# Kernel tuning notes

Hardware: AMD Instinct MI355X
Metric: run time of the kernel (lower is better)

## Reference

```python
import jax, jax.numpy as jnp
import numpy as np

N = 1_000_000
D = 128
B = 1024  # number of graphs in the batch


def setup_inputs() -> dict:
    key = jax.random.key(0)
    k1, k2, k3 = jax.random.split(key, 3)
    feat = jax.random.normal(k1, (N, D), dtype=jnp.float32)
    w_gate = jax.random.normal(k2, (D, 1), dtype=jnp.float32) * 0.02
    b_gate = jnp.zeros((1,), dtype=jnp.float32)
    segment_ids = jnp.sort(jax.random.randint(k3, (N,), 0, B, dtype=jnp.int32))
    return {"feat": feat, "w_gate": w_gate, "b_gate": b_gate,
            "segment_ids": segment_ids}


def reference(feat, w_gate, b_gate, segment_ids):
    # gate_nn: Linear(D, 1) -> per-node scalar score
    gate = (feat @ w_gate + b_gate)[:, 0]                      # [N]
    # softmax_nodes: per-graph (segment) numerically stable softmax
    seg_max = jax.ops.segment_max(gate, segment_ids, num_segments=B)   # [B]
    e = jnp.exp(gate - seg_max[segment_ids])                   # [N]
    seg_sum = jax.ops.segment_sum(e, segment_ids, num_segments=B)      # [B]
    alpha = e / seg_sum[segment_ids]                           # [N]
    # sum_nodes of feat * gate: weighted per-graph readout
    readout = jax.ops.segment_sum(feat * alpha[:, None], segment_ids,
                                  num_segments=B)              # [B, D]
    return readout, alpha[:, None]
```

## Files before the change

kernel.cpp:

```cpp
#include <hip/hip_runtime.h>
#include <math.h>

__global__ __launch_bounds__(256) void k_segstart(
        const int* __restrict__ seg, int* __restrict__ segstart, int N, int B) {
    int i = blockIdx.x * blockDim.x + threadIdx.x;
    if (i >= N) return;
    int s = seg[i];
    int p = (i == 0) ? -1 : seg[i - 1];
    for (int bb = p + 1; bb <= s; ++bb) segstart[bb] = i;
    if (i == N - 1)
        for (int bb = s + 1; bb <= B; ++bb) segstart[bb] = N;
}

__global__ __launch_bounds__(256) void k_pool(
        const float* __restrict__ feat, const float* __restrict__ w,
        const float* __restrict__ bptr, const int* __restrict__ segstart,
        float* __restrict__ gbuf, float* __restrict__ Mbuf,
        float* __restrict__ invbuf, float* __restrict__ readout) {
    int b = blockIdx.x;
    int start = segstart[b], end = segstart[b + 1];
    int t = threadIdx.x, rg = t >> 5, cl = t & 31;

    const float4 w4 = ((const float4*)w)[cl];
    const float bias = bptr[0];
    const float4* featv = (const float4*)feat;

    float m = -INFINITY, s = 0.0f;
    float4 acc = make_float4(0.0f, 0.0f, 0.0f, 0.0f);

    const int n0 = start + rg;

#define LDROW(dst, row)                                                       \
    dst = ((row) < end) ? featv[(size_t)(row) * 32 + cl]                      \
                        : make_float4(0.0f, 0.0f, 0.0f, 0.0f)

    float4 f0, f1, f2, f3;
    LDROW(f0, n0);
    LDROW(f1, n0 + 8);
    LDROW(f2, n0 + 16);
    LDROW(f3, n0 + 24);

#define UPDATE(v, f, row) do {                                                \
        if ((row) < end) {                                                    \
            float g = (v) + bias;                                             \
            if (cl == 0) gbuf[row] = g;                                       \
            float e;                                                          \
            if (g > m) {                                                      \
                float r = __expf(m - g);        \
                s *= r;                                                       \
                acc.x *= r; acc.y *= r; acc.z *= r; acc.w *= r;               \
                m = g; e = 1.0f;                                              \
            } else {                                                          \
                e = __expf(g - m);                                            \
            }                                                                 \
            s += e;                                                           \
            acc.x += f.x * e; acc.y += f.y * e;                               \
            acc.z += f.z * e; acc.w += f.w * e;                               \
        } } while (0)

    for (int n = n0; n < end; n += 32) {
        float4 p0, p1, p2, p3;
        LDROW(p0, n + 32);
        LDROW(p1, n + 40);
        LDROW(p2, n + 48);
        LDROW(p3, n + 56);

        float v0 = f0.x * w4.x + f0.y * w4.y + f0.z * w4.z + f0.w * w4.w;
        float v1 = f1.x * w4.x + f1.y * w4.y + f1.z * w4.z + f1.w * w4.w;
        float v2 = f2.x * w4.x + f2.y * w4.y + f2.z * w4.z + f2.w * w4.w;
        float v3 = f3.x * w4.x + f3.y * w4.y + f3.z * w4.z + f3.w * w4.w;
        #pragma unroll
        for (int d = 1; d < 32; d <<= 1) {
            v0 += __shfl_xor(v0, d);
            v1 += __shfl_xor(v1, d);
            v2 += __shfl_xor(v2, d);
            v3 += __shfl_xor(v3, d);
        }

        UPDATE(v0, f0, n);
        UPDATE(v1, f1, n + 8);
        UPDATE(v2, f2, n + 16);
        UPDATE(v3, f3, n + 24);

        f0 = p0; f1 = p1; f2 = p2; f3 = p3;
    }

    __shared__ float mred[8], sred[8];
    if (cl == 0) { mred[rg] = m; sred[rg] = s; }
    __syncthreads();
    float M = -INFINITY;
    #pragma unroll
    for (int g2 = 0; g2 < 8; ++g2) M = fmaxf(M, mred[g2]);
    float S = 0.0f;
    #pragma unroll
    for (int g2 = 0; g2 < 8; ++g2)
        if (sred[g2] > 0.0f) S += sred[g2] * __expf(mred[g2] - M);
    const float inv = (S > 0.0f) ? 1.0f / S : 0.0f;

    float r = (s > 0.0f) ? __expf(m - M) : 0.0f;
    acc.x *= r; acc.y *= r; acc.z *= r; acc.w *= r;

    __shared__ float4 red[256];
    red[t] = acc;
    __syncthreads();
    #pragma unroll
    for (int off = 4; off >= 1; off >>= 1) {
        if (rg < off) {
            float4 o = red[t + off * 32];
            red[t].x += o.x; red[t].y += o.y; red[t].z += o.z; red[t].w += o.w;
        }
        __syncthreads();
    }
    if (rg == 0) {
        float4 o = red[t];
        o.x *= inv; o.y *= inv; o.z *= inv; o.w *= inv;
        ((float4*)(readout + (size_t)b * 128))[cl] = o;
    }
    if (t == 0) { Mbuf[b] = M; invbuf[b] = inv; }
}

__global__ __launch_bounds__(256) void k_alpha(
        const float* __restrict__ gbuf, const int* __restrict__ seg,
        const float* __restrict__ Mbuf, const float* __restrict__ invbuf,
        float* __restrict__ alpha, int N) {
    int i = blockIdx.x * blockDim.x + threadIdx.x;
    int i4 = i * 4;
    if (i4 + 3 < N) {
        float4 g = ((const float4*)gbuf)[i];
        int4 sv = ((const int4*)seg)[i];
        float4 a;
        a.x = __expf(g.x - Mbuf[sv.x]) * invbuf[sv.x];
        a.y = __expf(g.y - Mbuf[sv.y]) * invbuf[sv.y];
        a.z = __expf(g.z - Mbuf[sv.z]) * invbuf[sv.z];
        a.w = __expf(g.w - Mbuf[sv.w]) * invbuf[sv.w];
        ((float4*)alpha)[i] = a;
    } else if (i4 < N) {
        for (int k = i4; k < N; ++k) {
            int sb = seg[k];
            alpha[k] = __expf(gbuf[k] - Mbuf[sb]) * invbuf[sb];
        }
    }
}

extern "C" void kernel_launch(void* const* d_in, const int* in_sizes, int n_in,
                              void* d_out, int out_size, void* d_ws, size_t ws_size,
                              hipStream_t stream) {
    const float* feat  = (const float*)d_in[0];
    const float* wgate = (const float*)d_in[1];
    const float* bgate = (const float*)d_in[2];
    const int*   seg   = (const int*)d_in[3];

    const int N = in_sizes[3];
    const int D = in_sizes[1];
    const int B = (out_size - N) / D;

    float* readout = (float*)d_out;
    float* alpha   = (float*)d_out + (size_t)B * 128;

    int* segstart = (int*)d_ws;
    size_t off = (((size_t)(B + 1) * 4) + 255) & ~(size_t)255;
    float* Mbuf = (float*)((char*)d_ws + off);
    float* invbuf = Mbuf + B;
    size_t off2 = (off + (size_t)2 * B * 4 + 255) & ~(size_t)255;
    float* gbuf = (float*)((char*)d_ws + off2);

    k_segstart<<<(N + 255) / 256, 256, 0, stream>>>(seg, segstart, N, B);
    k_pool<<<B, 256, 0, stream>>>(feat, wgate, bgate, segstart,
                                  gbuf, Mbuf, invbuf, readout);
    int threads4 = (N + 3) / 4;
    k_alpha<<<(threads4 + 255) / 256, 256, 0, stream>>>(gbuf, seg, Mbuf, invbuf,
                                                        alpha, N);
}
```

Measured before the change: 640.7 us.

## Process 8 rows per iteration with DPP reductions and batched online softmax

Rewrites the k_pool main loop so each row group handles 8 rows per step (64 rows per block iteration), with double-buffered float4 prefetch of 8 rows. The 32-lane dot-product reduction uses DPP row operations plus one ds_swizzle in place of shfl_xor. The online-softmax max rescale happens once per batch of 8 instead of once per row, and a simple remainder loop handles the tail. It also adds a minimum-blocks hint to launch_bounds. The goal is more memory-level parallelism and fewer reduction and branch instructions, at the cost of higher register pressure from holding 16 float4s per thread.

Result: slower. 665.6 us (+3.9%).

```diff
diff --git a/kernel.cpp b/kernel.cpp
--- a/kernel.cpp
+++ b/kernel.cpp
@@ -12,7 +12,22 @@
         for (int bb = s + 1; bb <= B; ++bb) segstart[bb] = N;
 }
 
-__global__ __launch_bounds__(256) void k_pool(
+template <int CTRL>
+__device__ __forceinline__ float dpp_add(float v) {
+    int sh = __builtin_amdgcn_update_dpp(0, __float_as_int(v), CTRL, 0xF, 0xF,
+                                         false);
+    return v + __int_as_float(sh);
+}
+__device__ __forceinline__ float halfwave_sum(float v) {
+    v = dpp_add<0xB1>(v);
+    v = dpp_add<0x4E>(v);
+    v = dpp_add<0x141>(v);
+    v = dpp_add<0x140>(v);
+    int sw = __builtin_amdgcn_ds_swizzle(__float_as_int(v), 0x401F);
+    return v + __int_as_float(sw);
+}
+
+__global__ __launch_bounds__(256, 4) void k_pool(
         const float* __restrict__ feat, const float* __restrict__ w,
         const float* __restrict__ bptr, const int* __restrict__ segstart,
         float* __restrict__ gbuf, float* __restrict__ Mbuf,
@@ -28,65 +43,88 @@
     float m = -INFINITY, s = 0.0f;
     float4 acc = make_float4(0.0f, 0.0f, 0.0f, 0.0f);
 
-    const int n0 = start + rg;
-
-#define LDROW(dst, row)                                                       \
-    dst = ((row) < end) ? featv[(size_t)(row) * 32 + cl]                      \
-                        : make_float4(0.0f, 0.0f, 0.0f, 0.0f)
-
-    float4 f0, f1, f2, f3;
-    LDROW(f0, n0);
-    LDROW(f1, n0 + 8);
-    LDROW(f2, n0 + 16);
-    LDROW(f3, n0 + 24);
-
-#define UPDATE(v, f, row) do {                                                \
-        if ((row) < end) {                                                    \
-            float g = (v) + bias;                                             \
-            if (cl == 0) gbuf[row] = g;                                       \
-            float e;                                                          \
-            if (g > m) {                                                      \
-                float r = __expf(m - g);        \
-                s *= r;                                                       \
-                acc.x *= r; acc.y *= r; acc.z *= r; acc.w *= r;               \
-                m = g; e = 1.0f;                                              \
-            } else {                                                          \
-                e = __expf(g - m);                                            \
-            }                                                                 \
-            s += e;                                                           \
-            acc.x += f.x * e; acc.y += f.y * e;                               \
-            acc.z += f.z * e; acc.w += f.w * e;                               \
-        } } while (0)
-
-    for (int n = n0; n < end; n += 32) {
-        float4 p0, p1, p2, p3;
-        LDROW(p0, n + 32);
-        LDROW(p1, n + 40);
-        LDROW(p2, n + 48);
-        LDROW(p3, n + 56);
-
-        float v0 = f0.x * w4.x + f0.y * w4.y + f0.z * w4.z + f0.w * w4.w;
-        float v1 = f1.x * w4.x + f1.y * w4.y + f1.z * w4.z + f1.w * w4.w;
-        float v2 = f2.x * w4.x + f2.y * w4.y + f2.z * w4.z + f2.w * w4.w;
-        float v3 = f3.x * w4.x + f3.y * w4.y + f3.z * w4.z + f3.w * w4.w;
+    const int len = end - start;
+    const int nfull = len >> 6;
+    const float4* rowp = featv + (size_t)(start + rg) * 32 + cl;
+    const bool cl0 = (cl == 0);
+
+    float4 f[8], p[8];
+
+#define PROCESS8(rowbase)                                                     \
+    do {                                                                      \
+        float g[8];                                                           \
+        _Pragma("unroll") for (int j = 0; j < 8; ++j)                         \
+            g[j] = f[j].x * w4.x + f[j].y * w4.y + f[j].z * w4.z +            \
+                   f[j].w * w4.w;                                             \
+        _Pragma("unroll") for (int j = 0; j < 8; ++j)                         \
+            g[j] = dpp_add<0xB1>(g[j]);                                       \
+        _Pragma("unroll") for (int j = 0; j < 8; ++j)                         \
+            g[j] = dpp_add<0x4E>(g[j]);                                       \
+        _Pragma("unroll") for (int j = 0; j < 8; ++j)                         \
+            g[j] = dpp_add<0x141>(g[j]);                                      \
+        _Pragma("unroll") for (int j = 0; j < 8; ++j)                         \
+            g[j] = dpp_add<0x140>(g[j]);                                      \
+        _Pragma("unroll") for (int j = 0; j < 8; ++j) {                       \
+            int sw = __builtin_amdgcn_ds_swizzle(__float_as_int(g[j]),        \
+                                                 0x401F);                     \
+            g[j] = g[j] + __int_as_float(sw) + bias;                          \
+        }                                                                     \
+        if (cl0) {                                                            \
+            _Pragma("unroll") for (int j = 0; j < 8; ++j)                     \
+                gbuf[(rowbase) + 8 * j] = g[j];                               \
+        }                                                                     \
+        float gm = fmaxf(fmaxf(fmaxf(g[0], g[1]), fmaxf(g[2], g[3])),         \
+                         fmaxf(fmaxf(g[4], g[5]), fmaxf(g[6], g[7])));        \
+        if (gm > m) {                                                         \
+            float r = __expf(m - gm);         \
+            s *= r;                                                           \
+            acc.x *= r; acc.y *= r; acc.z *= r; acc.w *= r;                   \
+            m = gm;                                                           \
+        }                                                                     \
+        float e[8];                                                           \
+        _Pragma("unroll") for (int j = 0; j < 8; ++j)                         \
+            e[j] = __expf(g[j] - m);                                          \
+        s += ((e[0] + e[1]) + (e[2] + e[3])) +                                \
+             ((e[4] + e[5]) + (e[6] + e[7]));                                 \
+        _Pragma("unroll") for (int j = 0; j < 8; ++j) {                       \
+            acc.x += f[j].x * e[j]; acc.y += f[j].y * e[j];                   \
+            acc.z += f[j].z * e[j]; acc.w += f[j].w * e[j];                   \
+        }                                                                     \
+    } while (0)
+
+    if (nfull > 0) {
         #pragma unroll
-        for (int d = 1; d < 32; d <<= 1) {
-            v0 += __shfl_xor(v0, d);
-            v1 += __shfl_xor(v1, d);
-            v2 += __shfl_xor(v2, d);
-            v3 += __shfl_xor(v3, d);
-        }
-
-        UPDATE(v0, f0, n);
-        UPDATE(v1, f1, n + 8);
-        UPDATE(v2, f2, n + 16);
-        UPDATE(v3, f3, n + 24);
-
-        f0 = p0; f1 = p1; f2 = p2; f3 = p3;
+        for (int j = 0; j < 8; ++j) f[j] = rowp[(size_t)j * 256];
+        for (int it = 1; it < nfull; ++it) {
+            const float4* nxt = rowp + (size_t)it * 2048;
+            #pragma unroll
+            for (int j = 0; j < 8; ++j) p[j] = nxt[(size_t)j * 256];
+            PROCESS8(start + rg + (it - 1) * 64);
+            #pragma unroll
+            for (int j = 0; j < 8; ++j) f[j] = p[j];
+        }
+        PROCESS8(start + rg + (nfull - 1) * 64);
+    }
+
+    for (int n = start + nfull * 64 + rg; n < end; n += 8) {
+        float4 ft = featv[(size_t)n * 32 + cl];
+        float g = halfwave_sum(ft.x * w4.x + ft.y * w4.y + ft.z * w4.z +
+                               ft.w * w4.w) + bias;
+        if (cl0) gbuf[n] = g;
+        if (g > m) {
+            float r = __expf(m - g);
+            s *= r;
+            acc.x *= r; acc.y *= r; acc.z *= r; acc.w *= r;
+            m = g;
+        }
+        float e = __expf(g - m);
+        s += e;
+        acc.x += ft.x * e; acc.y += ft.y * e; acc.z += ft.z * e;
+        acc.w += ft.w * e;
     }
 
     __shared__ float mred[8], sred[8];
-    if (cl == 0) { mred[rg] = m; sred[rg] = s; }
+    if (cl0) { mred[rg] = m; sred[rg] = s; }
     __syncthreads();
     float M = -INFINITY;
     #pragma unroll
```
